# Kernel tuning notes

Measured on AMD Instinct MI355X. Metric: run time of the kernel, lower is better.

The kernel has to match this reference:

```python
import jax, jax.numpy as jnp
import numpy as np

B, T, C = 2, 2048, 1024
H = 16
D = C // H
E = 16
K = 2
THETA = 10000.0
ALPHA = 0.01
EPS = 1e-5


def rmsnorm(x, w):
    ms = jnp.mean(jnp.square(x), axis=-1, keepdims=True)
    return x * jax.lax.rsqrt(ms + EPS) * w


def rope_cos_sin(t_len, dim):
    # matches precompute_freqs_cis: freqs = theta**(-2i/dim), angles = t * freqs
    freqs = 1.0 / THETA ** (jnp.arange(0, dim // 2, dtype=jnp.float32) * 2.0 / dim)
    ang = jnp.arange(t_len, dtype=jnp.float32)[:, None] * freqs[None, :]  # [T, D/2]
    return jnp.cos(ang), jnp.sin(ang)


def apply_rope(x, cos, sin):
    # x: [B,T,H,D]; complex rotation on consecutive pairs (view_as_complex semantics)
    xr = x.reshape(x.shape[:-1] + (D // 2, 2))
    x0, x1 = xr[..., 0], xr[..., 1]
    c = cos[None, :, None, :]
    s = sin[None, :, None, :]
    return jnp.stack([x0 * c - x1 * s, x0 * s + x1 * c], axis=-1).reshape(x.shape)


def mlp(x, wf, bf, wp, bp):
    return jax.nn.silu(x @ wf + bf) @ wp + bp


def setup_inputs() -> dict:
    key = jax.random.key(0)
    ks = jax.random.split(key, 16)
    s = 0.02
    return {
        'x': jax.random.normal(ks[0], (B, T, C), jnp.float32),
        'ln1_w': jax.random.normal(ks[1], (C,), jnp.float32),
        'ln2_w': jax.random.normal(ks[2], (C,), jnp.float32),
        'w_attn': jax.random.normal(ks[3], (C, 3 * C), jnp.float32) * s,
        'b_attn': jnp.zeros((3 * C,), jnp.float32),
        'w_proj': jax.random.normal(ks[4], (C, C), jnp.float32) * s,
        'b_proj': jnp.zeros((C,), jnp.float32),
        'gate_w': jax.random.normal(ks[5], (E, C), jnp.float32) * s,
        'gate_bias': jnp.zeros((E,), jnp.float32),
        'exp_wf': jax.random.normal(ks[6], (E, C, 2 * C), jnp.float32) * s,
        'exp_bf': jnp.zeros((E, 2 * C), jnp.float32),
        'exp_wp': jax.random.normal(ks[7], (E, 2 * C, C), jnp.float32) * s,
        'exp_bp': jnp.zeros((E, C), jnp.float32),
        'sh_wf': jax.random.normal(ks[8], (C, 2 * C), jnp.float32) * s,
        'sh_bf': jnp.zeros((2 * C,), jnp.float32),
        'sh_wp': jax.random.normal(ks[9], (2 * C, C), jnp.float32) * s,
        'sh_bp': jnp.zeros((C,), jnp.float32),
    }


def reference(x, ln1_w, ln2_w, w_attn, b_attn, w_proj, b_proj, gate_w, gate_bias,
              exp_wf, exp_bf, exp_wp, exp_bp, sh_wf, sh_bf, sh_wp, sh_bp):
    # ---- attention sub-block ----
    h = rmsnorm(x, ln1_w)
    qkv = h @ w_attn + b_attn  # [B,T,3C]
    q, k, v = jnp.split(qkv, 3, axis=-1)
    q = q.reshape(B, T, H, D)
    k = k.reshape(B, T, H, D)
    v = v.reshape(B, T, H, D)
    cos, sin = rope_cos_sin(T, D)
    q = apply_rope(q, cos, sin)
    k = apply_rope(k, cos, sin)
    scores = jnp.einsum('bqhd,bkhd->bhqk', q, k) / jnp.sqrt(jnp.float32(D))
    causal = jnp.tril(jnp.ones((T, T), dtype=bool))
    scores = jnp.where(causal, scores, -jnp.inf)
    attn = jax.nn.softmax(scores, axis=-1)
    y = jnp.einsum('bhqk,bkhd->bqhd', attn, v).reshape(B, T, C)
    x = x + y @ w_proj + b_proj
    # ---- MoE sub-block ----
    h = rmsnorm(x, ln2_w).reshape(-1, C)  # [N,C]
    N = h.shape[0]
    logits = h @ gate_w.T
    p = jax.nn.softmax(logits.astype(jnp.float32), axis=-1)  # original_scores [N,E]
    _, idx = jax.lax.top_k(p + gate_bias, K)  # topk on biased scores
    w_sel = jnp.take_along_axis(p, idx, axis=-1)  # weights from unbiased scores [N,K]
    onehot = jax.nn.one_hot(idx, E, dtype=p.dtype)  # [N,K,E]
    w_dense = jnp.sum(onehot * w_sel[..., None], axis=1)  # [N,E] combine weights
    counts = jnp.sum(onehot, axis=(0, 1))  # bincount
    f_i = counts * E / (K * N + 1e-6)
    expert_probs = p.mean(axis=0)
    lb_loss = ALPHA * jnp.sum(f_i * expert_probs)
    out = jnp.zeros_like(h)
    for i in range(E):  # fixed small expert count
        out = out + mlp(h, exp_wf[i], exp_bf[i], exp_wp[i], exp_bp[i]) * w_dense[:, i:i + 1]
    out = out + mlp(h, sh_wf, sh_bf, sh_wp, sh_bp)
    return x + out.reshape(B, T, C), lb_loss
```

## Files before the change

kernel.cpp:

```cpp
#include <hip/hip_runtime.h>

typedef __bf16 bf16x8 __attribute__((ext_vector_type(8)));
typedef short  short8 __attribute__((ext_vector_type(8)));
typedef float  f32x4  __attribute__((ext_vector_type(4)));
typedef unsigned short u16;

#define NTOK 4096
#define TSEQ 2048
#define CDIM 1024
#define NEXP 16

__device__ __forceinline__ u16 f2bf(float f){
  union { float f; unsigned u; } v; v.f = f;
  unsigned r = v.u + 0x7fffu + ((v.u >> 16) & 1u);
  return (u16)(r >> 16);
}
__device__ __forceinline__ float bf2f(u16 u){
  union { unsigned u; float f; } v; v.u = ((unsigned)u) << 16; return v.f;
}

__device__ __forceinline__ f32x4 mfma16(short8 a, short8 b, f32x4 c){
  return __builtin_amdgcn_mfma_f32_16x16x32_bf16(
      __builtin_bit_cast(bf16x8, a), __builtin_bit_cast(bf16x8, b), c, 0, 0, 0);
}

__device__ __forceinline__ void gload_lds16(const void* g, void* l){
  __builtin_amdgcn_global_load_lds((__attribute__((address_space(1))) void*)g,
                                   (__attribute__((address_space(3))) void*)l,
                                   16, 0, 0);
}

__device__ __forceinline__ void tp_body(const float* __restrict__ in, u16* __restrict__ out,
                                        int K, int N, int k0, int n0, u16* lds16, int tid)
{
  int tx = tid & 15;
#pragma unroll
  for (int p = 0; p < 2; ++p) {
    int q = (tid >> 4) + p * 16;
    int k = 2 * q;
    float4 v0 = *(const float4*)(in + (size_t)(k0 + k)     * N + n0 + tx * 4);
    float4 v1 = *(const float4*)(in + (size_t)(k0 + k + 1) * N + n0 + tx * 4);
    const float* a0 = (const float*)&v0;
    const float* a1 = (const float*)&v1;
#pragma unroll
    for (int i = 0; i < 4; ++i) {
      unsigned val = (unsigned)f2bf(a0[i]) | ((unsigned)f2bf(a1[i]) << 16);
      *(unsigned*)&lds16[(tx * 4 + i) * 66 + k] = val;
    }
  }
  __syncthreads();
#pragma unroll
  for (int p = 0; p < 2; ++p) {
    int n = (tid >> 3) + p * 32;
    int k8 = (tid & 7) * 8;
    const unsigned* l32 = (const unsigned*)&lds16[n * 66 + k8];
    uint4 o4;
    o4.x = l32[0]; o4.y = l32[1]; o4.z = l32[2]; o4.w = l32[3];
    *(uint4*)(out + (size_t)(n0 + n) * K + k0 + k8) = o4;
  }
}

__global__ void transpose_wattn_k(const float* __restrict__ in, u16* __restrict__ out)
{
  __shared__ u16 lds16[64 * 66];
  int r = blockIdx.x;
  int n0 = (r % 48) * 64, k0 = (r / 48) * 64;
  tp_body(in, out, 1024, 3072, k0, n0, lds16, threadIdx.x);
}

__global__ void rmsnorm_k(const float* __restrict__ x, const float* __restrict__ w,
                          u16* __restrict__ ob, float* __restrict__ of)
{
  int row = blockIdx.x, tid = threadIdx.x;
  const float4* xr = (const float4*)(x + (size_t)row * CDIM);
  float4 v = xr[tid];
  float ss = v.x*v.x + v.y*v.y + v.z*v.z + v.w*v.w;
  for (int d = 1; d < 64; d <<= 1) ss += __shfl_xor(ss, d);
  __shared__ float wacc[4];
  if ((tid & 63) == 0) wacc[tid >> 6] = ss;
  __syncthreads();
  float tot = wacc[0] + wacc[1] + wacc[2] + wacc[3];
  float scale = rsqrtf(tot * (1.0f / CDIM) + 1e-5f);
  float4 wv = ((const float4*)w)[tid];
  float o0 = v.x * scale * wv.x, o1 = v.y * scale * wv.y;
  float o2 = v.z * scale * wv.z, o3 = v.w * scale * wv.w;
  if (of) ((float4*)(of + (size_t)row * CDIM))[tid] = make_float4(o0, o1, o2, o3);
  ushort4 ov; ov.x = f2bf(o0); ov.y = f2bf(o1); ov.z = f2bf(o2); ov.w = f2bf(o3);
  ((ushort4*)(ob + (size_t)row * CDIM))[tid] = ov;
}

template<int MODE>
__global__ void __launch_bounds__(256, 4)
gemm_bt(const u16* __restrict__ A, int lda,
        const u16* __restrict__ Bt, long long bStrideZ,
        const float* __restrict__ bias, int biasStrideZ,
        void* __restrict__ Cout,
        const float* __restrict__ resid,
        int M, int N, int K,
        const int* __restrict__ counts, const int* __restrict__ offsets,
        const int* __restrict__ tokA)
{
  int nwg = gridDim.x * gridDim.y * gridDim.z;
  int d = (blockIdx.z * gridDim.y + blockIdx.y) * gridDim.x + blockIdx.x;
  int o = (d & 7) * (nwg >> 3) + (d >> 3);
  int cb = o % gridDim.x;
  int t2 = o / gridDim.x;
  int rb = t2 % gridDim.y;
  int z  = t2 / gridDim.y;

  int mLoc = M, rowBase = 0;
  if (counts) { mLoc = counts[z]; rowBase = offsets[z]; }
  if (rb * 128 >= mLoc) return;

  const u16* Bz = Bt + (size_t)z * bStrideZ;
  const float* bz = bias + (size_t)z * biasStrideZ;

  __shared__ u16 lds_a[2][128 * 32];
  __shared__ u16 lds_b[2][128 * 32];

  int tid = threadIdx.x;
  int lane = tid & 63, wave = tid >> 6;
  int wm = wave >> 1, wn = wave & 1;
  int srow = wave * 16 + (lane >> 2);
  int skel = (lane & 3) * 8;
  int r16 = lane & 15, g8 = (lane >> 4) * 8;

  size_t arow[2];
  int ncol[2];
#pragma unroll
  for (int c = 0; c < 2; ++c) {
    int rloc = rb * 128 + c * 64 + srow;
    if (rloc >= mLoc) rloc = mLoc - 1;
    int grow = rowBase + rloc;
    arow[c] = tokA ? (size_t)tokA[grow] : (size_t)grow;
    ncol[c] = cb * 128 + c * 64 + srow;
  }

  f32x4 acc[4][4] = {};

  auto stage = [&](int kt, int buf){
    int k0 = kt * 32;
#pragma unroll
    for (int c = 0; c < 2; ++c) {
      gload_lds16(A + arow[c] * lda + k0 + skel,
                  (char*)&lds_a[buf][0] + c * 4096 + wave * 1024);
      gload_lds16(Bz + (size_t)ncol[c] * K + k0 + skel,
                  (char*)&lds_b[buf][0] + c * 4096 + wave * 1024);
    }
  };

  int nkt = K >> 5;
  stage(0, 0);
  for (int kt = 0; kt < nkt; ++kt) {
    int buf = kt & 1;
    if (kt + 1 < nkt) {
      stage(kt + 1, buf ^ 1);
      asm volatile("s_waitcnt vmcnt(4)" ::: "memory");
    } else {
      asm volatile("s_waitcnt vmcnt(0)" ::: "memory");
    }
    __builtin_amdgcn_s_barrier();
    short8 af[4], bfr[4];
#pragma unroll
    for (int i = 0; i < 4; ++i) {
      af[i]  = *(const short8*)&lds_a[buf][(wm * 64 + i * 16 + r16) * 32 + g8];
      bfr[i] = *(const short8*)&lds_b[buf][(wn * 64 + i * 16 + r16) * 32 + g8];
    }
#pragma unroll
    for (int i = 0; i < 4; ++i)
#pragma unroll
      for (int j = 0; j < 4; ++j)
        acc[i][j] = mfma16(af[i], bfr[j], acc[i][j]);
    __builtin_amdgcn_s_barrier();
  }

#pragma unroll
  for (int i = 0; i < 4; ++i) {
    int rl0 = rb * 128 + wm * 64 + i * 16 + (lane >> 4) * 4;
#pragma unroll
    for (int j = 0; j < 4; ++j) {
      int col = cb * 128 + wn * 64 + j * 16 + r16;
      float bv = bz[col];
#pragma unroll
      for (int r = 0; r < 4; ++r) {
        int rl = rl0 + r;
        if (rl >= mLoc) continue;
        int grow = rowBase + rl;
        float v = acc[i][j][r] + bv;
        if (MODE == 0) {
          ((float*)Cout)[(size_t)grow * N + col] = v;
        } else if (MODE == 1) {
          ((float*)Cout)[(size_t)grow * N + col] = v + resid[(size_t)grow * N + col];
        } else if (MODE == 2) {
          float s = v * (1.0f / (1.0f + __expf(-v)));
          ((u16*)Cout)[(size_t)grow * N + col] = f2bf(s);
        } else {
          ((u16*)Cout)[(size_t)grow * N + col] = f2bf(v);
        }
      }
    }
  }
}

__global__ void rope_split_k(const float* __restrict__ qkv,
                             u16* __restrict__ qr, u16* __restrict__ kr,
                             u16* __restrict__ vt)
{
  int flat = blockIdx.x * 256 + threadIdx.x;
  int i = flat & 31;
  int h = (flat >> 5) & 15;
  int n = flat >> 9;
  int b = n >> 11, t = n & 2047;
  const float* row = qkv + (size_t)n * 3072;
  float2 q = *(const float2*)(row + h * 64 + 2 * i);
  float2 k = *(const float2*)(row + 1024 + h * 64 + 2 * i);
  float2 v = *(const float2*)(row + 2048 + h * 64 + 2 * i);
  float freq = expf(-(float)i * (2.0f / 64.0f) * 9.210340371976184f);
  float ang = (float)t * freq;
  float sn, cs;
  sincosf(ang, &sn, &cs);
  float q0 = q.x * cs - q.y * sn, q1 = q.x * sn + q.y * cs;
  float k0 = k.x * cs - k.y * sn, k1 = k.x * sn + k.y * cs;
  int bh = b * 16 + h;
  size_t qoff = ((size_t)bh * TSEQ + t) * 64 + 2 * i;
  *(unsigned*)(qr + qoff) = (unsigned)f2bf(q0) | ((unsigned)f2bf(q1) << 16);
  *(unsigned*)(kr + qoff) = (unsigned)f2bf(k0) | ((unsigned)f2bf(k1) << 16);
  size_t voff = ((size_t)bh * 64 + 2 * i) * TSEQ + t;
  vt[voff] = f2bf(v.x);
  vt[voff + TSEQ] = f2bf(v.y);
}

__global__ void __launch_bounds__(512, 4)
attn_tp_k(const u16* __restrict__ qr, const u16* __restrict__ kr,
          const u16* __restrict__ vt, u16* __restrict__ y,
          const float* __restrict__ wProj, const float* __restrict__ shWf,
          const float* __restrict__ shWp,  const float* __restrict__ expWf,
          const float* __restrict__ expWp,
          u16* __restrict__ oProj, u16* __restrict__ oWf17, u16* __restrict__ oWp17)
{
  __shared__ union {
    struct { u16 lK[2][64 * 64]; u16 lV[2][64 * 64]; u16 plds[8][16 * 72]; } a;
    u16 t[2][64 * 66];
  } sm;

  int u = blockIdx.x;
  if (u >= 512) {
    int tid = threadIdx.x;
    int half = tid >> 8, t256 = tid & 255;
    int t = (u - 512) * 2 + half;
    const float* in; u16* out; int K, N, k0, n0;
    if (t < 8192) {
      int z = t >> 9, r = t & 511;
      in = expWf + (size_t)z * 2048 * 1024; out = oWf17 + (size_t)z * 2048 * 1024;
      K = 1024; N = 2048; n0 = (r & 31) * 64; k0 = (r >> 5) * 64;
    } else if (t < 16384) {
      int z = (t - 8192) >> 9, r = (t - 8192) & 511;
      in = expWp + (size_t)z * 2048 * 1024; out = oWp17 + (size_t)z * 2048 * 1024;
      K = 2048; N = 1024; n0 = (r & 15) * 64; k0 = (r >> 4) * 64;
    } else if (t < 16896) {
      int r = t - 16384;
      in = shWf; out = oWf17 + (size_t)16 * 2048 * 1024;
      K = 1024; N = 2048; n0 = (r & 31) * 64; k0 = (r >> 5) * 64;
    } else if (t < 17408) {
      int r = t - 16896;
      in = shWp; out = oWp17 + (size_t)16 * 2048 * 1024;
      K = 2048; N = 1024; n0 = (r & 15) * 64; k0 = (r >> 4) * 64;
    } else {
      int r = t - 17408;
      in = wProj; out = oProj; K = 1024; N = 1024; n0 = (r & 15) * 64; k0 = (r >> 4) * 64;
    }
    tp_body(in, out, K, N, k0, n0, &sm.t[half][0], t256);
    return;
  }

  int bh = u >> 4;
  int b = bh >> 4, h = bh & 15;
  int qb = 15 - (u & 15);
  int tid = threadIdx.x;
  int wv = tid >> 6, lane = tid & 63;
  int qrow0 = qb * 128 + wv * 16;
  const u16* qbase = qr + (size_t)bh * TSEQ * 64;
  const u16* kbase = kr + (size_t)bh * TSEQ * 64;
  const u16* vbase = vt + (size_t)bh * 64 * TSEQ;

  u16* pw = &sm.a.plds[wv][0];

  int r16 = lane & 15, g = lane >> 4;

  short8 aq0 = *(const short8*)(qbase + (size_t)(qrow0 + r16) * 64 + g * 8);
  short8 aq1 = *(const short8*)(qbase + (size_t)(qrow0 + r16) * 64 + 32 + g * 8);

  int sRow = tid >> 3;
  int sColE = (((tid & 7) * 16) ^ ((sRow & 7) << 4)) >> 1;

  float m[4] = {-1e30f, -1e30f, -1e30f, -1e30f};
  float l[4] = {0.f, 0.f, 0.f, 0.f};
  f32x4 o[4] = {};

  int nt = 2 * qb + 2;

  auto stage = [&](int t, int buf){
    int kp = t * 64;
    gload_lds16(kbase + ((size_t)(kp + sRow) << 6) + sColE,
                (char*)&sm.a.lK[buf][0] + wv * 1024);
    gload_lds16(vbase + (size_t)sRow * TSEQ + kp + sColE,
                (char*)&sm.a.lV[buf][0] + wv * 1024);
  };

  auto compute = [&](int t, int buf){
    int kp = t * 64;
    f32x4 s[4];
    __builtin_amdgcn_s_setprio(1);
#pragma unroll
    for (int st = 0; st < 4; ++st) {
      int rowK = st * 16 + r16;
      int sw = (rowK & 7) << 4;
      short8 kb0 = *(const short8*)((const char*)&sm.a.lK[buf][0] + rowK * 128 + ((g * 16) ^ sw));
      short8 kb1 = *(const short8*)((const char*)&sm.a.lK[buf][0] + rowK * 128 + ((64 + g * 16) ^ sw));
      f32x4 acc = {0.f, 0.f, 0.f, 0.f};
      acc = mfma16(aq0, kb0, acc);
      acc = mfma16(aq1, kb1, acc);
      s[st] = acc;
    }
    __builtin_amdgcn_s_setprio(0);

    float sc[4];
#pragma unroll
    for (int r = 0; r < 4; ++r) {
      int qpos = qrow0 + g * 4 + r;
      float v0 = (kp + r16      <= qpos) ? s[0][r] * 0.125f : -1e30f;
      float v1 = (kp + 16 + r16 <= qpos) ? s[1][r] * 0.125f : -1e30f;
      float v2 = (kp + 32 + r16 <= qpos) ? s[2][r] * 0.125f : -1e30f;
      float v3 = (kp + 48 + r16 <= qpos) ? s[3][r] * 0.125f : -1e30f;
      float mx = fmaxf(fmaxf(v0, v1), fmaxf(v2, v3));
      for (int d = 1; d < 16; d <<= 1) mx = fmaxf(mx, __shfl_xor(mx, d));
      float mnew = fmaxf(m[r], mx);
      float e0 = __expf(v0 - mnew), e1 = __expf(v1 - mnew);
      float e2 = __expf(v2 - mnew), e3 = __expf(v3 - mnew);
      float scale = __expf(m[r] - mnew);
      float rs = (e0 + e1) + (e2 + e3);
      for (int d = 1; d < 16; d <<= 1) rs += __shfl_xor(rs, d);
      l[r] = l[r] * scale + rs;
      m[r] = mnew;
      sc[r] = scale;
      int prow = (g * 4 + r) * 72;
      pw[prow + r16]      = f2bf(e0);
      pw[prow + 16 + r16] = f2bf(e1);
      pw[prow + 32 + r16] = f2bf(e2);
      pw[prow + 48 + r16] = f2bf(e3);
    }
#pragma unroll
    for (int c = 0; c < 4; ++c) {
      f32x4 t4 = o[c];
      t4[0] *= sc[0]; t4[1] *= sc[1]; t4[2] *= sc[2]; t4[3] *= sc[3];
      o[c] = t4;
    }

    short8 pa0 = *(const short8*)&pw[r16 * 72 + g * 8];
    short8 pa1 = *(const short8*)&pw[r16 * 72 + 32 + g * 8];
    __builtin_amdgcn_s_setprio(1);
#pragma unroll
    for (int c = 0; c < 4; ++c) {
      int rowV = c * 16 + r16;
      int sw = (rowV & 7) << 4;
      short8 vb0 = *(const short8*)((const char*)&sm.a.lV[buf][0] + rowV * 128 + ((g * 16) ^ sw));
      short8 vb1 = *(const short8*)((const char*)&sm.a.lV[buf][0] + rowV * 128 + ((64 + g * 16) ^ sw));
      o[c] = mfma16(pa0, vb0, o[c]);
      o[c] = mfma16(pa1, vb1, o[c]);
    }
    __builtin_amdgcn_s_setprio(0);
  };

  stage(0, 0);
  for (int t = 0; t < nt; ++t) {
    int buf = t & 1;
    if (t + 1 < nt) {
      stage(t + 1, buf ^ 1);
      asm volatile("s_waitcnt vmcnt(2)" ::: "memory");
    } else {
      asm volatile("s_waitcnt vmcnt(0)" ::: "memory");
    }
    __builtin_amdgcn_s_barrier();
    compute(t, buf);
    __builtin_amdgcn_s_barrier();
  }

#pragma unroll
  for (int c = 0; c < 4; ++c)
#pragma unroll
    for (int r = 0; r < 4; ++r) {
      int qpos = qrow0 + g * 4 + r;
      float val = o[c][r] / l[r];
      y[((size_t)(b * TSEQ + qpos)) * CDIM + h * 64 + c * 16 + r16] = f2bf(val);
    }
}

__global__ void zero_k(int* counts){
  int t = threadIdx.x;
  if (t < NEXP) counts[t] = 0;
}

__global__ void gate_k(const float* __restrict__ h2, const float* __restrict__ gw,
                       const float* __restrict__ gb,
                       int* __restrict__ route_e, float* __restrict__ route_w,
                       int* __restrict__ counts, float* __restrict__ probs)
{
  int n = blockIdx.x, tid = threadIdx.x;
  __shared__ float hrow[CDIM];
  __shared__ float part[16][17];
  __shared__ float sm[16];
  ((float4*)hrow)[tid] = ((const float4*)(h2 + (size_t)n * CDIM))[tid];
  __syncthreads();
  int e = tid & 15, seg = tid >> 4;
  const float4* gw4 = (const float4*)(gw + (size_t)e * CDIM + seg * 64);
  const float4* hs4 = (const float4*)(hrow + seg * 64);
  float p = 0.f;
#pragma unroll
  for (int i = 0; i < 16; ++i) {
    float4 gv = gw4[i];
    float4 hv = hs4[i];
    p += hv.x * gv.x;
    p += hv.y * gv.y;
    p += hv.z * gv.z;
    p += hv.w * gv.w;
  }
  part[e][seg] = p;
  __syncthreads();
  if (tid < 16) {
    float lg = 0.f;
    for (int s = 0; s < 16; ++s) lg += part[tid][s];
    sm[tid] = lg;
  }
  __syncthreads();
  if (tid == 0) {
    float mx = sm[0];
    for (int i = 1; i < 16; ++i) mx = fmaxf(mx, sm[i]);
    float ssum = 0.f;
    for (int i = 0; i < 16; ++i) { float pe = expf(sm[i] - mx); sm[i] = pe; ssum += pe; }
    float inv = 1.0f / ssum;
    for (int i = 0; i < 16; ++i) sm[i] *= inv;
    int i1 = -1; float b1 = -1e30f;
    for (int i = 0; i < 16; ++i) { float t = sm[i] + gb[i]; if (t > b1) { b1 = t; i1 = i; } }
    int i2 = -1; float b2 = -1e30f;
    for (int i = 0; i < 16; ++i) { if (i == i1) continue; float t = sm[i] + gb[i]; if (t > b2) { b2 = t; i2 = i; } }
    route_e[2 * n] = i1; route_e[2 * n + 1] = i2;
    route_w[2 * n] = sm[i1]; route_w[2 * n + 1] = sm[i2];
    atomicAdd(&counts[i1], 1); atomicAdd(&counts[i2], 1);
  }
  __syncthreads();
  if (tid < 16) probs[(size_t)n * 16 + tid] = sm[tid];
}

__global__ void scan_k(const int* counts, int* offs, int* cursors){
  if (threadIdx.x == 0) {
    int acc = 0;
    for (int e = 0; e < NEXP; ++e) { offs[e] = acc; cursors[e] = acc; acc += counts[e]; }
    offs[NEXP] = acc;
  }
}

__global__ void fill_k(const int* __restrict__ route_e, const float* __restrict__ route_w,
                       int* __restrict__ cursors, int* __restrict__ tok, float* __restrict__ tw,
                       int* __restrict__ inv)
{
  int n = blockIdx.x * 256 + threadIdx.x;
  if (n >= NTOK) return;
  for (int j = 0; j < 2; ++j) {
    int e = route_e[2 * n + j];
    int pos = atomicAdd(&cursors[e], 1);
    tok[pos] = n; tw[pos] = route_w[2 * n + j];
    inv[2 * n + j] = pos;
  }
}

__global__ void combine_k(float* __restrict__ out, const u16* __restrict__ eout,
                          const int* __restrict__ inv, const float* __restrict__ tw)
{
  int n = blockIdx.x, tid = threadIdx.x;
  int p0 = inv[2 * n], p1 = inv[2 * n + 1];
  float w0 = tw[p0], w1 = tw[p1];
  float4 a  = ((float4*)(out + (size_t)n * CDIM))[tid];
  ushort4 e0 = ((const ushort4*)(eout + (size_t)p0 * CDIM))[tid];
  ushort4 e1 = ((const ushort4*)(eout + (size_t)p1 * CDIM))[tid];
  a.x += bf2f(e0.x) * w0 + bf2f(e1.x) * w1;
  a.y += bf2f(e0.y) * w0 + bf2f(e1.y) * w1;
  a.z += bf2f(e0.z) * w0 + bf2f(e1.z) * w1;
  a.w += bf2f(e0.w) * w0 + bf2f(e1.w) * w1;
  ((float4*)(out + (size_t)n * CDIM))[tid] = a;
}

__global__ void lb2_k(const int* __restrict__ counts, const float* __restrict__ probs,
                      float* __restrict__ out)
{
  __shared__ float part[256][16];
  int t = threadIdx.x;
  float acc[16];
#pragma unroll
  for (int e = 0; e < 16; ++e) acc[e] = 0.f;
  for (int n = t; n < NTOK; n += 256) {
    const float4* row = (const float4*)(probs + (size_t)n * 16);
    float4 a0 = row[0], a1 = row[1], a2 = row[2], a3 = row[3];
    acc[0] += a0.x; acc[1] += a0.y; acc[2]  += a0.z; acc[3]  += a0.w;
    acc[4] += a1.x; acc[5] += a1.y; acc[6]  += a1.z; acc[7]  += a1.w;
    acc[8] += a2.x; acc[9] += a2.y; acc[10] += a2.z; acc[11] += a2.w;
    acc[12] += a3.x; acc[13] += a3.y; acc[14] += a3.z; acc[15] += a3.w;
  }
#pragma unroll
  for (int e = 0; e < 16; ++e) part[t][e] = acc[e];
  __syncthreads();
  __shared__ float colsum[16];
  if (t < 16) {
    float s = 0.f;
    for (int i = 0; i < 256; ++i) s += part[i][t];
    colsum[t] = s;
  }
  __syncthreads();
  if (t == 0) {
    float accl = 0.f;
    for (int e = 0; e < NEXP; ++e) {
      float f = (float)counts[e] * (16.0f / (2.0f * (float)NTOK + 1e-6f));
      accl += f * (colsum[e] * (1.0f / (float)NTOK));
    }
    out[0] = 0.01f * accl;
  }
}

extern "C" void kernel_launch(void* const* d_in, const int* in_sizes, int n_in,
                              void* d_out, int out_size, void* d_ws, size_t ws_size,
                              hipStream_t stream)
{
  const float* x      = (const float*)d_in[0];
  const float* ln1_w  = (const float*)d_in[1];
  const float* ln2_w  = (const float*)d_in[2];
  const float* w_attn = (const float*)d_in[3];
  const float* b_attn = (const float*)d_in[4];
  const float* w_proj = (const float*)d_in[5];
  const float* b_proj = (const float*)d_in[6];
  const float* gate_w = (const float*)d_in[7];
  const float* gate_b = (const float*)d_in[8];
  const float* exp_wf = (const float*)d_in[9];
  const float* exp_bf = (const float*)d_in[10];
  const float* exp_wp = (const float*)d_in[11];
  const float* exp_bp = (const float*)d_in[12];
  const float* sh_wf  = (const float*)d_in[13];
  const float* sh_bf  = (const float*)d_in[14];
  const float* sh_wp  = (const float*)d_in[15];
  const float* sh_bp  = (const float*)d_in[16];

  char* ws = (char*)d_ws;
  size_t off = 0;
  auto alloc = [&](size_t b){ size_t r = off; off = (off + b + 255) & ~(size_t)255; return r; };

  size_t oWAttnT = alloc(3072ull * 1024 * 2);
  size_t oWProjT = alloc(1024ull * 1024 * 2);
  size_t oExpWfT = alloc(17ull * 2048 * 1024 * 2);
  size_t oExpWpT = alloc(17ull * 1024 * 2048 * 2);
  size_t oX2     = alloc(4096ull * 1024 * 4);
  size_t oH2F    = alloc(4096ull * 2048 * 2);
  size_t oH2B    = alloc(4096ull * 1024 * 2);
  size_t oQKV    = alloc(4096ull * 3072 * 4);
  size_t oQR     = alloc(4096ull * 1024 * 2);
  size_t oKR     = alloc(4096ull * 1024 * 2);
  size_t oVT     = alloc(4096ull * 1024 * 2);
  size_t oH1B    = alloc(4096ull * 1024 * 2);
  size_t oCnt    = alloc(128);
  size_t oOffs   = alloc(128);
  size_t oCurs   = alloc(128);
  size_t oRE     = alloc(8192ull * 4);
  size_t oRW     = alloc(8192ull * 4);
  size_t oTok    = alloc(8192ull * 4);
  size_t oTw     = alloc(8192ull * 4);
  size_t oInv    = alloc(8192ull * 4);
  size_t oProbs  = alloc(4096ull * 16 * 4);

  u16* pWAttnT = (u16*)(ws + oWAttnT);
  u16* pWProjT = (u16*)(ws + oWProjT);
  u16* pWf17   = (u16*)(ws + oExpWfT);
  u16* pWp17   = (u16*)(ws + oExpWpT);
  float* pX2   = (float*)(ws + oX2);
  float* pH2F  = (float*)(ws + oH2F);
  u16* pHidSh  = (u16*)(ws + oH2F);
  u16* pH2B    = (u16*)(ws + oH2B);
  float* pQKV  = (float*)(ws + oQKV);
  u16* pHidMoe = (u16*)(ws + oQKV);
  u16* pQR     = (u16*)(ws + oQR);
  u16* pKR     = (u16*)(ws + oKR);
  u16* pVT     = (u16*)(ws + oVT);
  u16* pH1B    = (u16*)(ws + oH1B);
  u16* pY      = (u16*)(ws + oH1B);
  u16* pEoutB  = (u16*)(ws + oQR);
  int* pCnt    = (int*)(ws + oCnt);
  int* pOffs   = (int*)(ws + oOffs);
  int* pCurs   = (int*)(ws + oCurs);
  int* pRE     = (int*)(ws + oRE);
  float* pRW   = (float*)(ws + oRW);
  int* pTok    = (int*)(ws + oTok);
  float* pTw   = (float*)(ws + oTw);
  int* pInv    = (int*)(ws + oInv);
  float* pProbs= (float*)(ws + oProbs);

  transpose_wattn_k<<<768, 256, 0, stream>>>(w_attn, pWAttnT);

  rmsnorm_k<<<NTOK, 256, 0, stream>>>(x, ln1_w, pH1B, nullptr);

  gemm_bt<0><<<dim3(3072/128, NTOK/128, 1), 256, 0, stream>>>(
      pH1B, 1024, pWAttnT, 0, b_attn, 0, pQKV, nullptr,
      NTOK, 3072, 1024, nullptr, nullptr, nullptr);

  rope_split_k<<<(NTOK * 16 * 32) / 256, 256, 0, stream>>>(pQKV, pQR, pKR, pVT);

  attn_tp_k<<<512 + 8832, 512, 0, stream>>>(pQR, pKR, pVT, pY,
                                            w_proj, sh_wf, sh_wp, exp_wf, exp_wp,
                                            pWProjT, pWf17, pWp17);

  gemm_bt<1><<<dim3(1024/128, NTOK/128, 1), 256, 0, stream>>>(
      pY, 1024, pWProjT, 0, b_proj, 0, pX2, x,
      NTOK, 1024, 1024, nullptr, nullptr, nullptr);

  rmsnorm_k<<<NTOK, 256, 0, stream>>>(pX2, ln2_w, pH2B, pH2F);

  zero_k<<<1, 64, 0, stream>>>(pCnt);
  gate_k<<<NTOK, 256, 0, stream>>>(pH2F, gate_w, gate_b, pRE, pRW, pCnt, pProbs);
  scan_k<<<1, 64, 0, stream>>>(pCnt, pOffs, pCurs);
  fill_k<<<NTOK/256, 256, 0, stream>>>(pRE, pRW, pCurs, pTok, pTw, pInv);
  lb2_k<<<1, 256, 0, stream>>>(pCnt, pProbs, ((float*)d_out) + (size_t)NTOK * CDIM);

  gemm_bt<2><<<dim3(2048/128, NTOK/128, 1), 256, 0, stream>>>(
      pH2B, 1024, pWf17 + (size_t)16 * 2048 * 1024, 0, sh_bf, 0, pHidSh, nullptr,
      NTOK, 2048, 1024, nullptr, nullptr, nullptr);

  gemm_bt<1><<<dim3(1024/128, NTOK/128, 1), 256, 0, stream>>>(
      pHidSh, 2048, pWp17 + (size_t)16 * 2048 * 1024, 0, sh_bp, 0, (float*)d_out, pX2,
      NTOK, 1024, 2048, nullptr, nullptr, nullptr);

  gemm_bt<2><<<dim3(2048/128, NTOK/128, 16), 256, 0, stream>>>(
      pH2B, 1024, pWf17, 2048ll * 1024, exp_bf, 2048, pHidMoe, nullptr,
      NTOK, 2048, 1024, pCnt, pOffs, pTok);

  gemm_bt<4><<<dim3(1024/128, NTOK/128, 16), 256, 0, stream>>>(
      pHidMoe, 2048, pWp17, 2048ll * 1024, exp_bp, 1024, pEoutB, nullptr,
      NTOK, 1024, 2048, pCnt, pOffs, nullptr);

  combine_k<<<NTOK, 256, 0, stream>>>((float*)d_out, pEoutB, pInv, pTw);

  (void)in_sizes; (void)n_in; (void)out_size; (void)ws_size;
}
```

Before: 672.2 us.

## Fold shared expert into grouped MoE GEMMs and fuse V transpose into QKV epilogue

Treats the shared MLP as a 17th expert covering all tokens, so one grouped GEMM launch per MoE layer handles both. Biases are concatenated into 17-slot buffers, and combine_k now sums the residual, the shared-expert output and the routed outputs in one pass. The QKV GEMM epilogue writes V directly in transposed bf16 layout, so the rope kernel only processes Q and K. The grouped GEMMs drop the XCD block swizzle, and the shared-expert output is now rounded to bf16 before combine, which slightly changes precision.

```diff
diff --git a/kernel.cpp b/kernel.cpp
--- a/kernel.cpp
+++ b/kernel.cpp
@@ -66,6 +66,17 @@
   int r = blockIdx.x;
   int n0 = (r % 48) * 64, k0 = (r / 48) * 64;
   tp_body(in, out, 1024, 3072, k0, n0, lds16, threadIdx.x);
+}
+
+__global__ void concat_bias_k(const float* __restrict__ exp_bf, const float* __restrict__ sh_bf,
+                              const float* __restrict__ exp_bp, const float* __restrict__ sh_bp,
+                              float* __restrict__ bf17, float* __restrict__ bp17)
+{
+  int i = blockIdx.x * 256 + threadIdx.x;
+  if (i < 16 * 2048) bf17[i] = exp_bf[i];
+  else if (i < 17 * 2048) bf17[i] = sh_bf[i - 16 * 2048];
+  if (i < 16 * 1024) bp17[i] = exp_bp[i];
+  else if (i < 17 * 1024) bp17[i] = sh_bp[i - 16 * 1024];
 }
 
 __global__ void rmsnorm_k(const float* __restrict__ x, const float* __restrict__ w,
@@ -89,7 +100,7 @@
   ((ushort4*)(ob + (size_t)row * CDIM))[tid] = ov;
 }
 
-template<int MODE>
+template<int MODE, int SWZ>
 __global__ void __launch_bounds__(256, 4)
 gemm_bt(const u16* __restrict__ A, int lda,
         const u16* __restrict__ Bt, long long bStrideZ,
@@ -98,15 +109,20 @@
         const float* __restrict__ resid,
         int M, int N, int K,
         const int* __restrict__ counts, const int* __restrict__ offsets,
-        const int* __restrict__ tokA)
-{
-  int nwg = gridDim.x * gridDim.y * gridDim.z;
-  int d = (blockIdx.z * gridDim.y + blockIdx.y) * gridDim.x + blockIdx.x;
-  int o = (d & 7) * (nwg >> 3) + (d >> 3);
-  int cb = o % gridDim.x;
-  int t2 = o / gridDim.x;
-  int rb = t2 % gridDim.y;
-  int z  = t2 / gridDim.y;
+        const int* __restrict__ tokA, u16* __restrict__ vtp)
+{
+  int cb, rb, z;
+  if (SWZ) {
+    int nwg = gridDim.x * gridDim.y * gridDim.z;
+    int d = (blockIdx.z * gridDim.y + blockIdx.y) * gridDim.x + blockIdx.x;
+    int o = (d & 7) * (nwg >> 3) + (d >> 3);
+    cb = o % gridDim.x;
+    int t2 = o / gridDim.x;
+    rb = t2 % gridDim.y;
+    z  = t2 / gridDim.y;
+  } else {
+    cb = blockIdx.x; rb = blockIdx.y; z = blockIdx.z;
+  }
 
   int mLoc = M, rowBase = 0;
   if (counts) { mLoc = counts[z]; rowBase = offsets[z]; }
@@ -194,17 +210,25 @@
         } else if (MODE == 2) {
           float s = v * (1.0f / (1.0f + __expf(-v)));
           ((u16*)Cout)[(size_t)grow * N + col] = f2bf(s);
+        } else if (MODE == 4) {
+          ((u16*)Cout)[(size_t)grow * N + col] = f2bf(v);
         } else {
-          ((u16*)Cout)[(size_t)grow * N + col] = f2bf(v);
+          if (col < 2048) {
+            ((float*)Cout)[(size_t)grow * N + col] = v;
+          } else {
+            int c10 = col - 2048;
+            int h = c10 >> 6, dd = c10 & 63;
+            int b = grow >> 11, t = grow & 2047;
+            vtp[((size_t)(b * 16 + h) * 64 + dd) * TSEQ + t] = f2bf(v);
+          }
         }
       }
     }
   }
 }
 
-__global__ void rope_split_k(const float* __restrict__ qkv,
-                             u16* __restrict__ qr, u16* __restrict__ kr,
-                             u16* __restrict__ vt)
+__global__ void rope_qk_k(const float* __restrict__ qkv,
+                          u16* __restrict__ qr, u16* __restrict__ kr)
 {
   int flat = blockIdx.x * 256 + threadIdx.x;
   int i = flat & 31;
@@ -214,7 +238,6 @@
   const float* row = qkv + (size_t)n * 3072;
   float2 q = *(const float2*)(row + h * 64 + 2 * i);
   float2 k = *(const float2*)(row + 1024 + h * 64 + 2 * i);
-  float2 v = *(const float2*)(row + 2048 + h * 64 + 2 * i);
   float freq = expf(-(float)i * (2.0f / 64.0f) * 9.210340371976184f);
   float ang = (float)t * freq;
   float sn, cs;
@@ -225,9 +248,6 @@
   size_t qoff = ((size_t)bh * TSEQ + t) * 64 + 2 * i;
   *(unsigned*)(qr + qoff) = (unsigned)f2bf(q0) | ((unsigned)f2bf(q1) << 16);
   *(unsigned*)(kr + qoff) = (unsigned)f2bf(k0) | ((unsigned)f2bf(k1) << 16);
-  size_t voff = ((size_t)bh * 64 + 2 * i) * TSEQ + t;
-  vt[voff] = f2bf(v.x);
-  vt[voff + TSEQ] = f2bf(v.y);
 }
 
 __global__ void __launch_bounds__(512, 4)
@@ -398,6 +418,7 @@
 __global__ void zero_k(int* counts){
   int t = threadIdx.x;
   if (t < NEXP) counts[t] = 0;
+  if (t == NEXP) counts[NEXP] = NTOK;
 }
 
 __global__ void gate_k(const float* __restrict__ h2, const float* __restrict__ gw,
@@ -471,15 +492,23 @@
     tok[pos] = n; tw[pos] = route_w[2 * n + j];
     inv[2 * n + j] = pos;
   }
-}
-
-__global__ void combine_k(float* __restrict__ out, const u16* __restrict__ eout,
+  tok[2 * NTOK + n] = n;
+}
+
+__global__ void combine_k(float* __restrict__ out, const float* __restrict__ x2,
+                          const u16* __restrict__ eout,
                           const int* __restrict__ inv, const float* __restrict__ tw)
 {
   int n = blockIdx.x, tid = threadIdx.x;
   int p0 = inv[2 * n], p1 = inv[2 * n + 1];
   float w0 = tw[p0], w1 = tw[p1];
-  float4 a  = ((float4*)(out + (size_t)n * CDIM))[tid];
+  float4 xr = ((const float4*)(x2 + (size_t)n * CDIM))[tid];
+  ushort4 es = ((const ushort4*)(eout + (size_t)(2 * NTOK + n) * CDIM))[tid];
+  float4 a;
+  a.x = xr.x + bf2f(es.x);
+  a.y = xr.y + bf2f(es.y);
+  a.z = xr.z + bf2f(es.z);
+  a.w = xr.w + bf2f(es.w);
   ushort4 e0 = ((const ushort4*)(eout + (size_t)p0 * CDIM))[tid];
   ushort4 e1 = ((const ushort4*)(eout + (size_t)p1 * CDIM))[tid];
   a.x += bf2f(e0.x) * w0 + bf2f(e1.x) * w1;
@@ -556,7 +585,7 @@
   size_t oExpWfT = alloc(17ull * 2048 * 1024 * 2);
   size_t oExpWpT = alloc(17ull * 1024 * 2048 * 2);
   size_t oX2     = alloc(4096ull * 1024 * 4);
-  size_t oH2F    = alloc(4096ull * 2048 * 2);
+  size_t oH2F    = alloc(4096ull * 1024 * 4);
   size_t oH2B    = alloc(4096ull * 1024 * 2);
   size_t oQKV    = alloc(4096ull * 3072 * 4);
   size_t oQR     = alloc(4096ull * 1024 * 2);
@@ -568,10 +597,12 @@
   size_t oCurs   = alloc(128);
   size_t oRE     = alloc(8192ull * 4);
   size_t oRW     = alloc(8192ull * 4);
-  size_t oTok    = alloc(8192ull * 4);
+  size_t oTok    = alloc(12288ull * 4);
   size_t oTw     = alloc(8192ull * 4);
   size_t oInv    = alloc(8192ull * 4);
   size_t oProbs  = alloc(4096ull * 16 * 4);
+  size_t oBf17   = alloc(17ull * 2048 * 4);
+  size_t oBp17   = alloc(17ull * 1024 * 4);
 
   u16* pWAttnT = (u16*)(ws + oWAttnT);
   u16* pWProjT = (u16*)(ws + oWProjT);
@@ -579,10 +610,9 @@
   u16* pWp17   = (u16*)(ws + oExpWpT);
   float* pX2   = (float*)(ws + oX2);
   float* pH2F  = (float*)(ws + oH2F);
-  u16* pHidSh  = (u16*)(ws + oH2F);
   u16* pH2B    = (u16*)(ws + oH2B);
   float* pQKV  = (float*)(ws + oQKV);
-  u16* pHidMoe = (u16*)(ws + oQKV);
+  u16* pHid17  = (u16*)(ws + oQKV);
   u16* pQR     = (u16*)(ws + oQR);
   u16* pKR     = (u16*)(ws + oKR);
   u16* pVT     = (u16*)(ws + oVT);
@@ -598,24 +628,27 @@
   float* pTw   = (float*)(ws + oTw);
   int* pInv    = (int*)(ws + oInv);
   float* pProbs= (float*)(ws + oProbs);
+  float* pBf17 = (float*)(ws + oBf17);
+  float* pBp17 = (float*)(ws + oBp17);
 
   transpose_wattn_k<<<768, 256, 0, stream>>>(w_attn, pWAttnT);
+  concat_bias_k<<<(17 * 2048 + 255) / 256, 256, 0, stream>>>(exp_bf, sh_bf, exp_bp, sh_bp, pBf17, pBp17);
 
   rmsnorm_k<<<NTOK, 256, 0, stream>>>(x, ln1_w, pH1B, nullptr);
 
-  gemm_bt<0><<<dim3(3072/128, NTOK/128, 1), 256, 0, stream>>>(
+  gemm_bt<5, 1><<<dim3(3072/128, NTOK/128, 1), 256, 0, stream>>>(
       pH1B, 1024, pWAttnT, 0, b_attn, 0, pQKV, nullptr,
-      NTOK, 3072, 1024, nullptr, nullptr, nullptr);
-
-  rope_split_k<<<(NTOK * 16 * 32) / 256, 256, 0, stream>>>(pQKV, pQR, pKR, pVT);
+      NTOK, 3072, 1024, nullptr, nullptr, nullptr, pVT);
+
+  rope_qk_k<<<(NTOK * 16 * 32) / 256, 256, 0, stream>>>(pQKV, pQR, pKR);
 
   attn_tp_k<<<512 + 8832, 512, 0, stream>>>(pQR, pKR, pVT, pY,
                                             w_proj, sh_wf, sh_wp, exp_wf, exp_wp,
                                             pWProjT, pWf17, pWp17);
 
-  gemm_bt<1><<<dim3(1024/128, NTOK/128, 1), 256, 0, stream>>>(
+  gemm_bt<1, 1><<<dim3(1024/128, NTOK/128, 1), 256, 0, stream>>>(
       pY, 1024, pWProjT, 0, b_proj, 0, pX2, x,
-      NTOK, 1024, 1024, nullptr, nullptr, nullptr);
+      NTOK, 1024, 1024, nullptr, nullptr, nullptr, nullptr);
 
   rmsnorm_k<<<NTOK, 256, 0, stream>>>(pX2, ln2_w, pH2B, pH2F);
 
@@ -625,23 +658,15 @@
   fill_k<<<NTOK/256, 256, 0, stream>>>(pRE, pRW, pCurs, pTok, pTw, pInv);
   lb2_k<<<1, 256, 0, stream>>>(pCnt, pProbs, ((float*)d_out) + (size_t)NTOK * CDIM);
 
-  gemm_bt<2><<<dim3(2048/128, NTOK/128, 1), 256, 0, stream>>>(
-      pH2B, 1024, pWf17 + (size_t)16 * 2048 * 1024, 0, sh_bf, 0, pHidSh, nullptr,
-      NTOK, 2048, 1024, nullptr, nullptr, nullptr);
-
-  gemm_bt<1><<<dim3(1024/128, NTOK/128, 1), 256, 0, stream>>>(
-      pHidSh, 2048, pWp17 + (size_t)16 * 2048 * 1024, 0, sh_bp, 0, (float*)d_out, pX2,
-      NTOK, 1024, 2048, nullptr, nullptr, nullptr);
-
-  gemm_bt<2><<<dim3(2048/128, NTOK/128, 16), 256, 0, stream>>>(
-      pH2B, 1024, pWf17, 2048ll * 1024, exp_bf, 2048, pHidMoe, nullptr,
-      NTOK, 2048, 1024, pCnt, pOffs, pTok);
-
-  gemm_bt<4><<<dim3(1024/128, NTOK/128, 16), 256, 0, stream>>>(
-      pHidMoe, 2048, pWp17, 2048ll * 1024, exp_bp, 1024, pEoutB, nullptr,
-      NTOK, 1024, 2048, pCnt, pOffs, nullptr);
-
-  combine_k<<<NTOK, 256, 0, stream>>>((float*)d_out, pEoutB, pInv, pTw);
+  gemm_bt<2, 0><<<dim3(2048/128, NTOK/128, 17), 256, 0, stream>>>(
+      pH2B, 1024, pWf17, 2048ll * 1024, pBf17, 2048, pHid17, nullptr,
+      NTOK, 2048, 1024, pCnt, pOffs, pTok, nullptr);
+
+  gemm_bt<4, 0><<<dim3(1024/128, NTOK/128, 17), 256, 0, stream>>>(
+      pHid17, 2048, pWp17, 2048ll * 1024, pBp17, 1024, pEoutB, nullptr,
+      NTOK, 1024, 2048, pCnt, pOffs, nullptr, nullptr);
+
+  combine_k<<<NTOK, 256, 0, stream>>>((float*)d_out, pX2, pEoutB, pInv, pTw);
 
   (void)in_sizes; (void)n_in; (void)out_size; (void)ws_size;
 }
```

Result: faster. 636.7 us (-5.3%).
